# Kernel optimization log

Measured on AMD Instinct MI355X. Metric: run time of the kernel, lower is better.

The kernel has to match this reference:

```python
import jax, jax.numpy as jnp
import numpy as np

B, N = 64, 4096
D_IN, D_SLOT, K, N_ITER, MLP_H = 128, 128, 8, 3, 256
EPS = 1e-8
LN_EPS = 1e-5  # torch LayerNorm default


def layer_norm(x, g, b):
    m = jnp.mean(x, axis=-1, keepdims=True)
    v = jnp.mean((x - m) ** 2, axis=-1, keepdims=True)
    return (x - m) * jax.lax.rsqrt(v + LN_EPS) * g + b


def setup_inputs() -> dict:
    key = jax.random.key(0)
    ks = jax.random.split(key, 12)
    s = D_SLOT ** -0.5
    return {
        "inputs": jax.random.normal(ks[0], (B, N, D_IN), jnp.float32),
        "noise": jax.random.normal(ks[1], (B, K, D_SLOT), jnp.float32),
        "ln_in_g": jnp.ones((D_IN,), jnp.float32),
        "ln_in_b": jnp.zeros((D_IN,), jnp.float32),
        "ln_sl_g": jnp.ones((D_SLOT,), jnp.float32),
        "ln_sl_b": jnp.zeros((D_SLOT,), jnp.float32),
        "ln_mlp_g": jnp.ones((D_SLOT,), jnp.float32),
        "ln_mlp_b": jnp.zeros((D_SLOT,), jnp.float32),
        "slots_mu": jax.random.normal(ks[2], (1, 1, D_SLOT), jnp.float32) * s,
        "slots_log_sigma": jnp.zeros((1, 1, D_SLOT), jnp.float32),
        "Wq": jax.random.normal(ks[3], (D_SLOT, D_SLOT), jnp.float32) * s,
        "Wk": jax.random.normal(ks[4], (D_SLOT, D_IN), jnp.float32) * s,
        "Wv": jax.random.normal(ks[5], (D_SLOT, D_IN), jnp.float32) * s,
        "gru_Wih": jax.random.normal(ks[6], (3 * D_SLOT, D_SLOT), jnp.float32) * s,
        "gru_Whh": jax.random.normal(ks[7], (3 * D_SLOT, D_SLOT), jnp.float32) * s,
        "gru_bih": jnp.zeros((3 * D_SLOT,), jnp.float32),
        "gru_bhh": jnp.zeros((3 * D_SLOT,), jnp.float32),
        "mlp_W1": jax.random.normal(ks[8], (MLP_H, D_SLOT), jnp.float32) * s,
        "mlp_b1": jnp.zeros((MLP_H,), jnp.float32),
        "mlp_W2": jax.random.normal(ks[9], (D_SLOT, MLP_H), jnp.float32) * (MLP_H ** -0.5),
        "mlp_b2": jnp.zeros((D_SLOT,), jnp.float32),
    }


def gru_cell(x, h, Wih, Whh, bih, bhh):
    # torch GRUCell: gate order r, z, n
    gx = x @ Wih.T + bih
    gh = h @ Whh.T + bhh
    xr, xz, xn = jnp.split(gx, 3, axis=-1)
    hr, hz, hn = jnp.split(gh, 3, axis=-1)
    r = jax.nn.sigmoid(xr + hr)
    z = jax.nn.sigmoid(xz + hz)
    n = jnp.tanh(xn + r * hn)
    return (1.0 - z) * n + z * h


def reference(inputs, noise, ln_in_g, ln_in_b, ln_sl_g, ln_sl_b, ln_mlp_g, ln_mlp_b,
              slots_mu, slots_log_sigma, Wq, Wk, Wv,
              gru_Wih, gru_Whh, gru_bih, gru_bhh,
              mlp_W1, mlp_b1, mlp_W2, mlp_b2):
    # init slots: mu + sigma * eps
    slots = slots_mu + jnp.exp(slots_log_sigma) * noise  # (B, K, d)
    x = layer_norm(inputs, ln_in_g, ln_in_b)
    k = jnp.einsum('bnd,ed->bne', x, Wk)  # (B, N, d_slot)
    v = jnp.einsum('bnd,ed->bne', x, Wv)
    scale = D_SLOT ** -0.5
    attn = None
    for _ in range(N_ITER):
        slots_prev = slots
        s_n = layer_norm(slots, ln_sl_g, ln_sl_b)
        q = jnp.einsum('bkd,ed->bke', s_n, Wq)
        dots = jnp.einsum('bkd,bnd->bkn', q, k) * scale
        attn = jax.nn.softmax(dots, axis=1)  # competitive: softmax over slots
        attn_normed = attn / (jnp.sum(attn, axis=-1, keepdims=True) + EPS)
        updates = jnp.einsum('bkn,bnd->bkd', attn_normed, v)
        slots = gru_cell(updates.reshape(-1, D_SLOT), slots_prev.reshape(-1, D_SLOT),
                         gru_Wih, gru_Whh, gru_bih, gru_bhh).reshape(B, K, D_SLOT)
        h = layer_norm(slots, ln_mlp_g, ln_mlp_b)
        h = jax.nn.gelu(h @ mlp_W1.T + mlp_b1, approximate=False)
        slots = slots + h @ mlp_W2.T + mlp_b2
    return slots, attn
```

## Files before the change

### kernel.cpp

```cpp
#include <hip/hip_runtime.h>
#include <hip/hip_bf16.h>
#include <math.h>

typedef unsigned int u32;
typedef unsigned long long u64;
typedef unsigned short u16;
typedef __bf16 bf16x8 __attribute__((ext_vector_type(8)));
typedef float f32x4 __attribute__((ext_vector_type(4)));

#define DEV __device__ __forceinline__

DEV u32 bfr(float f){ u32 u = __float_as_uint(f); return (u + 0x7fffu + ((u>>16)&1u)) >> 16; }
DEV u16 b1v(float a){ return __builtin_bit_cast(u16, (__bf16)a); }
DEV u32 pk2(float a, float b){
  return (u32)__builtin_bit_cast(u16, (__bf16)a) | ((u32)__builtin_bit_cast(u16, (__bf16)b) << 16);
}
DEV float red32(float v){
  v += __shfl_xor(v,1); v += __shfl_xor(v,2); v += __shfl_xor(v,4);
  v += __shfl_xor(v,8); v += __shfl_xor(v,16); return v;
}

__global__ void kInitSlots(const float* __restrict__ noise, const float* __restrict__ mu,
                           const float* __restrict__ ls, float* __restrict__ slots){
  int i4 = blockIdx.x*256 + threadIdx.x;
  int d4 = i4 & 31;
  float4 nv = ((const float4*)noise)[i4];
  float4 mv = ((const float4*)mu)[d4];
  float4 lv = ((const float4*)ls)[d4];
  float4 r;
  r.x = mv.x + expf(lv.x)*nv.x;
  r.y = mv.y + expf(lv.y)*nv.y;
  r.z = mv.z + expf(lv.z)*nv.z;
  r.w = mv.w + expf(lv.w)*nv.w;
  ((float4*)slots)[i4] = r;
}

__global__ void kInitW(const float* __restrict__ Wk, const float* __restrict__ Wv,
                       const float* __restrict__ g, const float* __restrict__ bb,
                       u16* __restrict__ wg, float* __restrict__ c1, float* __restrict__ c2){
  int e = threadIdx.x;
  const float4* src = (const float4*)((e < 128) ? (Wk + e*128) : (Wv + (e-128)*128));
  float a1 = 0.f, a2 = 0.f;
  #pragma unroll
  for (int d4 = 0; d4 < 32; ++d4){
    float4 wv = src[d4];
    float4 gv = ((const float4*)g)[d4];
    float4 bv = ((const float4*)bb)[d4];
    a1 += wv.x*gv.x + wv.y*gv.y + wv.z*gv.z + wv.w*gv.w;
    a2 += wv.x*bv.x + wv.y*bv.y + wv.z*bv.z + wv.w*bv.w;
    u32 w0 = bfr(wv.x*gv.x) | (bfr(wv.y*gv.y) << 16);
    u32 w1 = bfr(wv.z*gv.z) | (bfr(wv.w*gv.w) << 16);
    *(uint2*)&wg[e*128 + d4*4] = make_uint2(w0, w1);
  }
  c1[e] = a1; c2[e] = a2;
}

__global__ void kInitT(const float* __restrict__ Wih, const float* __restrict__ Whh,
                       const float* __restrict__ W1, const float* __restrict__ W2,
                       float2* __restrict__ gruT, float* __restrict__ w1T, float* __restrict__ w2T){
  int i = blockIdx.x*256 + threadIdx.x;
  if (i < 49152){
    int d = i / 384, g = i - d*384;
    gruT[i] = make_float2(Wih[g*128 + d], Whh[g*128 + d]);
  } else if (i < 81920){
    int j = i - 49152;
    int d = j >> 8, h = j & 255;
    w1T[j] = W1[h*128 + d];
  } else if (i < 114688){
    int q = i - 81920;
    int j = q >> 7, d = q & 127;
    w2T[q] = W2[d*256 + j];
  }
}

__global__ __launch_bounds__(512, 2) void kA(const float* __restrict__ x,
    const u16* __restrict__ wg, const float* __restrict__ c1g, const float* __restrict__ c2g,
    u16* __restrict__ kbuf, u16* __restrict__ vbuf)
{
  __shared__ __align__(16) u16 sWg[128*128];
  __shared__ __align__(16) u16 sE[8*16*128];
  __shared__ float sC1[128], sC2[128];
  const int t = threadIdx.x, l = t & 63, w = t >> 6;
  const int bid = blockIdx.x;
  const int half = (bid >> 3) & 1;
  const int sub  = (bid >> 4) & 1;
  const int rowgroup = (bid & 7)*32 + (bid >> 5);
  const int rowbase = rowgroup * 1024;

  const uint4* wg4 = (const uint4*)wg;
  #pragma unroll
  for (int p = 0; p < 4; ++p){
    int G = t + p*512;
    int row = G >> 4, g = G & 15;
    uint4 v = wg4[(half*128 + row)*16 + g];
    *(uint4*)&sWg[row*128 + ((g ^ (row & 7)) << 3)] = v;
  }
  if (t < 128){ sC1[t] = c1g[half*128 + t]; sC2[t] = c2g[half*128 + t]; }
  __syncthreads();

  u16* dstbuf = half ? vbuf : kbuf;
  const float4* x4 = (const float4*)x;

  #pragma unroll 1
  for (int s = sub*4; s < sub*4 + 4; ++s){
    const int r0 = rowbase + s*128 + w*16;
    const int myrow = r0 + (l & 15);
    float s1 = 0.f, s2 = 0.f;
    uint4 af[4];
    #pragma unroll
    for (int kt = 0; kt < 4; ++kt){
      int g = kt*4 + (l >> 4);
      float4 A = x4[(size_t)myrow*32 + g*2];
      float4 B = x4[(size_t)myrow*32 + g*2 + 1];
      s1 += A.x + A.y + A.z + A.w + B.x + B.y + B.z + B.w;
      s2 += A.x*A.x + A.y*A.y + A.z*A.z + A.w*A.w
          + B.x*B.x + B.y*B.y + B.z*B.z + B.w*B.w;
      af[kt].x = pk2(A.x, A.y);
      af[kt].y = pk2(A.z, A.w);
      af[kt].z = pk2(B.x, B.y);
      af[kt].w = pk2(B.z, B.w);
    }
    s1 += __shfl_xor(s1, 16); s2 += __shfl_xor(s2, 16);
    s1 += __shfl_xor(s1, 32); s2 += __shfl_xor(s2, 32);
    float m = s1 * 0.0078125f;
    float rstd = rsqrtf(s2 * 0.0078125f - m*m + 1e-5f);
    f32x4 acc[8];
    #pragma unroll
    for (int c_ = 0; c_ < 8; ++c_) acc[c_] = (f32x4){0.f,0.f,0.f,0.f};
    #pragma unroll
    for (int ct = 0; ct < 8; ++ct){
      uint4 bf[4];
      #pragma unroll
      for (int kt = 0; kt < 4; ++kt){
        int wr = ct*16 + (l & 15);
        int g = kt*4 + (l >> 4);
        bf[kt] = *(const uint4*)&sWg[wr*128 + ((g ^ (wr & 7)) << 3)];
      }
      #pragma unroll
      for (int kt = 0; kt < 4; ++kt)
        acc[ct] = __builtin_amdgcn_mfma_f32_16x16x32_bf16(
            __builtin_bit_cast(bf16x8, af[kt]),
            __builtin_bit_cast(bf16x8, bf[kt]),
            acc[ct], 0, 0, 0);
    }
    float mvp[4], rvp[4];
    #pragma unroll
    for (int r = 0; r < 4; ++r){
      int rl = (l >> 4)*4 + r;
      mvp[r] = __shfl(m, rl);
      rvp[r] = __shfl(rstd, rl);
    }
    #pragma unroll
    for (int ct = 0; ct < 8; ++ct){
      int col = ct*16 + (l & 15);
      float c1v = sC1[col], c2v = sC2[col];
      #pragma unroll
      for (int r = 0; r < 4; ++r){
        int rl = (l >> 4)*4 + r;
        float valf = rvp[r]*(acc[ct][r] - mvp[r]*c1v) + c2v;
        int gran = (col >> 3) ^ (rl & 7);
        sE[w*2048 + rl*128 + (gran << 3) + (col & 7)] = b1v(valf);
      }
    }
    uint4* dst4 = (uint4*)dstbuf;
    #pragma unroll
    for (int p = 0; p < 4; ++p){
      int fl = l + p*64;
      int nl = fl >> 4, gb = fl & 15;
      uint4 v = *(const uint4*)&sE[w*2048 + nl*128 + ((gb ^ (nl & 7)) << 3)];
      dst4[(size_t)(r0 + nl)*16 + gb] = v;
    }
  }
}

__global__ __launch_bounds__(256) void kQ(const float* __restrict__ slots,
    const float* __restrict__ Wq, const float* __restrict__ lng, const float* __restrict__ lnb,
    uint4* __restrict__ qg)
{
  const int b = blockIdx.x, t = threadIdx.x;
  const int k8 = t >> 5, q32 = t & 31;
  __shared__ __align__(16) float sSn[1024];
  __shared__ __align__(16) float sQ[1024];
  {
    float4 sv = ((const float4*)slots)[b*256 + t];
    float s  = sv.x + sv.y + sv.z + sv.w;
    float ss = sv.x*sv.x + sv.y*sv.y + sv.z*sv.z + sv.w*sv.w;
    s = red32(s); ss = red32(ss);
    float m = s*0.0078125f, var = ss*0.0078125f - m*m;
    float rstd = rsqrtf(var + 1e-5f);
    float4 gv = ((const float4*)lng)[q32], bv = ((const float4*)lnb)[q32];
    float4 sn;
    sn.x = (sv.x - m)*rstd*gv.x + bv.x;
    sn.y = (sv.y - m)*rstd*gv.y + bv.y;
    sn.z = (sv.z - m)*rstd*gv.z + bv.z;
    sn.w = (sv.w - m)*rstd*gv.w + bv.w;
    *(float4*)&sSn[t*4] = sn;
  }
  __syncthreads();
  {
    const float4* Wq4 = (const float4*)Wq;
    #pragma unroll
    for (int i = 0; i < 4; ++i){
      int e = i*32 + q32;
      float acc = 0.f;
      #pragma unroll
      for (int d4 = 0; d4 < 32; ++d4){
        float4 qs = *(const float4*)&sSn[k8*128 + d4*4];
        float4 wv = Wq4[e*32 + d4];
        acc = fmaf(qs.x,wv.x,acc); acc = fmaf(qs.y,wv.y,acc);
        acc = fmaf(qs.z,wv.z,acc); acc = fmaf(qs.w,wv.w,acc);
      }
      sQ[k8*128 + e] = acc * 0.08838834764831845f;
    }
  }
  __syncthreads();
  if (t < 128){
    int slot = t >> 4, g = t & 15;
    const float* src = &sQ[slot*128 + g*8];
    uint4 o;
    o.x = pk2(src[0], src[1]); o.y = pk2(src[2], src[3]);
    o.z = pk2(src[4], src[5]); o.w = pk2(src[6], src[7]);
    qg[(b*8 + slot)*16 + g] = o;
  }
}

__global__ __launch_bounds__(256) void kB(const u16* __restrict__ kbuf,
   const u16* __restrict__ vbuf, const uint4* __restrict__ qg,
   float* __restrict__ part, float* __restrict__ attn_out, int write_attn,
   int cshift, int ntiles)
{
  const int t = threadIdx.x;
  const int b = blockIdx.x >> cshift, chunk = blockIdx.x & ((1 << cshift) - 1);
  const int w = t >> 6, l = t & 63;
  __shared__ __align__(16) u16 sVT[128*64];
  __shared__ __align__(16) u16 sAttnB[16*64];
  __shared__ float sRsP[32];

  uint4 qf[4];
  {
    int slot = l & 15;
    uint4 z = make_uint4(0,0,0,0);
    qf[0] = z; qf[1] = z; qf[2] = z; qf[3] = z;
    if (slot < 8){
      const uint4* qb = qg + ((size_t)b*8 + slot)*16 + (l >> 4);
      #pragma unroll
      for (int kt = 0; kt < 4; ++kt) qf[kt] = qb[kt*4];
    }
  }

  f32x4 accPV0 = (f32x4){0.f,0.f,0.f,0.f};
  f32x4 accPV1 = (f32x4){0.f,0.f,0.f,0.f};
  float rs = 0.f;
  const int myrow = w*16 + (l & 15);
  const size_t base = (size_t)b*4096 + (size_t)chunk*(ntiles*64);

  uint4 kf[4], vld[4];
  {
    const u16* kr = kbuf + (base + myrow)*128;
    #pragma unroll
    for (int kt = 0; kt < 4; ++kt) kf[kt] = *(const uint4*)(kr + (kt*4 + (l >> 4))*8);
    const uint4* vg = (const uint4*)(vbuf + base*128);
    #pragma unroll
    for (int p = 0; p < 4; ++p) vld[p] = vg[t + p*256];
  }

  #pragma unroll 1
  for (int tile = 0; tile < ntiles; ++tile){
    const int n0 = tile*64;
    f32x4 dacc = (f32x4){0.f,0.f,0.f,0.f};
    #pragma unroll
    for (int kt = 0; kt < 4; ++kt)
      dacc = __builtin_amdgcn_mfma_f32_16x16x32_bf16(
          __builtin_bit_cast(bf16x8, kf[kt]),
          __builtin_bit_cast(bf16x8, qf[kt]), dacc, 0, 0, 0);
    uint4 vldN[4];
    if (tile < ntiles - 1){
      const u16* kr = kbuf + (base + n0 + 64 + myrow)*128;
      #pragma unroll
      for (int kt = 0; kt < 4; ++kt) kf[kt] = *(const uint4*)(kr + (kt*4 + (l >> 4))*8);
      const uint4* vg = (const uint4*)(vbuf + (base + n0 + 64)*128);
      #pragma unroll
      for (int p = 0; p < 4; ++p) vldN[p] = vg[t + p*256];
    }
    float at[4];
    #pragma unroll
    for (int r = 0; r < 4; ++r){
      float d = dacc[r];
      float mx = fmaxf(d, __shfl_xor(d, 1));
      mx = fmaxf(mx, __shfl_xor(mx, 2));
      mx = fmaxf(mx, __shfl_xor(mx, 4));
      float e = expf(d - mx);
      float ssum = e + __shfl_xor(e, 1);
      ssum += __shfl_xor(ssum, 2);
      ssum += __shfl_xor(ssum, 4);
      at[r] = e / ssum;
      rs += at[r];
    }
    {
      int slot = l & 15;
      int nb = w*16 + (l >> 4)*4;
      int g = (nb >> 3) ^ (slot & 7);
      *(u64*)((char*)sAttnB + slot*128 + (g << 4) + ((nb & 7) << 1)) =
          ((u64)pk2(at[2], at[3]) << 32) | (u64)pk2(at[0], at[1]);
    }
    #pragma unroll
    for (int p = 0; p < 4; ++p){
      int fl = t + p*256;
      int nl = fl >> 4, gb = fl & 15;
      u32 arr[4] = {vld[p].x, vld[p].y, vld[p].z, vld[p].w};
      #pragma unroll
      for (int h = 0; h < 4; ++h){
        #pragma unroll
        for (int e2 = 0; e2 < 2; ++e2){
          int e = h*2 + e2;
          int d = gb*8 + e;
          int g = (nl >> 3) ^ (d & 7) ^ (gb & 7);
          *(u16*)((char*)sVT + d*128 + (g << 4) + ((nl & 7) << 1)) =
              (u16)(e2 ? (arr[h] >> 16) : (arr[h] & 0xffffu));
        }
      }
    }
    if (write_attn && (l & 15) < 8){
      #pragma unroll
      for (int r = 0; r < 4; ++r)
        attn_out[(size_t)(b*8 + (l & 15))*4096 + chunk*(ntiles*64) + n0 + w*16 + (l >> 4)*4 + r] = at[r];
    }
    __syncthreads();
    #pragma unroll
    for (int step = 0; step < 2; ++step){
      uint4 paf;
      {
        int slot = l & 15;
        int g = (step*4 + (l >> 4)) ^ (slot & 7);
        paf = *(const uint4*)((const char*)sAttnB + slot*128 + (g << 4));
      }
      #pragma unroll
      for (int ct = 0; ct < 2; ++ct){
        int d = w*32 + ct*16 + (l & 15);
        int g = (step*4 + (l >> 4)) ^ (d & 7) ^ ((d >> 3) & 7);
        uint4 pbf = *(const uint4*)((const char*)sVT + d*128 + (g << 4));
        if (ct == 0)
          accPV0 = __builtin_amdgcn_mfma_f32_16x16x32_bf16(
              __builtin_bit_cast(bf16x8, paf), __builtin_bit_cast(bf16x8, pbf), accPV0, 0,0,0);
        else
          accPV1 = __builtin_amdgcn_mfma_f32_16x16x32_bf16(
              __builtin_bit_cast(bf16x8, paf), __builtin_bit_cast(bf16x8, pbf), accPV1, 0,0,0);
      }
    }
    __syncthreads();
    if (tile < ntiles - 1){
      #pragma unroll
      for (int p = 0; p < 4; ++p) vld[p] = vldN[p];
    }
  }

  float* pb = part + (size_t)blockIdx.x*1040;
  if ((l >> 4) < 2){
    #pragma unroll
    for (int r = 0; r < 4; ++r){
      int slot = (l >> 4)*4 + r;
      pb[slot*128 + w*32 + (l & 15)] = accPV0[r];
      pb[slot*128 + w*32 + 16 + (l & 15)] = accPV1[r];
    }
  }
  rs += __shfl_xor(rs, 16);
  rs += __shfl_xor(rs, 32);
  if (l < 8) sRsP[w*8 + l] = rs;
  __syncthreads();
  if (t < 8) pb[1024 + t] = sRsP[t] + sRsP[8 + t] + sRsP[16 + t] + sRsP[24 + t];
}

__global__ __launch_bounds__(384) void kC(const float* __restrict__ part,
  float* __restrict__ slots, const float2* __restrict__ gruT,
  const float* __restrict__ bih, const float* __restrict__ bhh,
  const float* __restrict__ lng, const float* __restrict__ lnb,
  const float* __restrict__ w1T, const float* __restrict__ b1,
  const float* __restrict__ w2T, const float* __restrict__ b2,
  const float* __restrict__ lnslg, const float* __restrict__ lnslb,
  const float* __restrict__ Wq, uint4* __restrict__ qg,
  float* __restrict__ out_slots, int last, int nchunk)
{
  const int t = threadIdx.x;
  const int r = blockIdx.x, b = r >> 3, k = r & 7;
  __shared__ float sU[128], sS[128], sG1[384], sG2[384];
  __shared__ float sNew[128], sH[128], sH1[256];
  __shared__ float sP[4];

  if (t < 128){
    float rs = 1e-8f;
    for (int c = 0; c < nchunk; ++c) rs += part[(size_t)(b*nchunk + c)*1040 + 1024 + k];
    float u = 0.f;
    for (int c = 0; c < nchunk; ++c) u += part[(size_t)(b*nchunk + c)*1040 + k*128 + t];
    sU[t] = u / rs;
    sS[t] = slots[r*128 + t];
  }
  __syncthreads();

  {
    float acc1 = bih[t], acc2 = bhh[t];
    #pragma unroll 8
    for (int d = 0; d < 128; ++d){
      float2 w = gruT[d*384 + t];
      float ud = sU[d], sd = sS[d];
      acc1 = fmaf(ud, w.x, acc1);
      acc2 = fmaf(sd, w.y, acc2);
    }
    sG1[t] = acc1; sG2[t] = acc2;
  }
  __syncthreads();

  if (t < 128){
    float rr = 1.f/(1.f + expf(-(sG1[t] + sG2[t])));
    float zz = 1.f/(1.f + expf(-(sG1[128 + t] + sG2[128 + t])));
    float nn = tanhf(sG1[256 + t] + rr*sG2[256 + t]);
    sNew[t] = (1.f - zz)*nn + zz*sS[t];
  }
  __syncthreads();
  if (t < 128){
    float v = sNew[t];
    float s = v, ss = v*v;
    s  += __shfl_xor(s,1);  ss += __shfl_xor(ss,1);
    s  += __shfl_xor(s,2);  ss += __shfl_xor(ss,2);
    s  += __shfl_xor(s,4);  ss += __shfl_xor(ss,4);
    s  += __shfl_xor(s,8);  ss += __shfl_xor(ss,8);
    s  += __shfl_xor(s,16); ss += __shfl_xor(ss,16);
    s  += __shfl_xor(s,32); ss += __shfl_xor(ss,32);
    if ((t & 63) == 0){ sP[(t >> 6)*2] = s; sP[(t >> 6)*2 + 1] = ss; }
  }
  __syncthreads();
  if (t < 128){
    float s = sP[0] + sP[2], ss = sP[1] + sP[3];
    float m = s*0.0078125f, var = ss*0.0078125f - m*m;
    float rstd = rsqrtf(var + 1e-5f);
    sH[t] = (sNew[t] - m)*rstd*lng[t] + lnb[t];
  }
  __syncthreads();

  if (t < 256){
    float acc = b1[t];
    #pragma unroll 8
    for (int d = 0; d < 128; ++d)
      acc = fmaf(sH[d], w1T[d*256 + t], acc);
    sH1[t] = 0.5f*acc*(1.f + erff(acc*0.70710678118654752f));
  }
  __syncthreads();

  float res = 0.f;
  if (t < 128){
    float acc = b2[t];
    #pragma unroll 8
    for (int j = 0; j < 256; ++j)
      acc = fmaf(sH1[j], w2T[j*128 + t], acc);
    res = sNew[t] + acc;
    slots[r*128 + t] = res;
    if (last) out_slots[r*128 + t] = res;
  }
  if (last) return;

  __syncthreads();
  if (t < 128) sH[t] = res;
  __syncthreads();
  if (t < 128){
    float v = sH[t];
    float s = v, ss = v*v;
    s  += __shfl_xor(s,1);  ss += __shfl_xor(ss,1);
    s  += __shfl_xor(s,2);  ss += __shfl_xor(ss,2);
    s  += __shfl_xor(s,4);  ss += __shfl_xor(ss,4);
    s  += __shfl_xor(s,8);  ss += __shfl_xor(ss,8);
    s  += __shfl_xor(s,16); ss += __shfl_xor(ss,16);
    s  += __shfl_xor(s,32); ss += __shfl_xor(ss,32);
    if ((t & 63) == 0){ sP[(t >> 6)*2] = s; sP[(t >> 6)*2 + 1] = ss; }
  }
  __syncthreads();
  if (t < 128){
    float s = sP[0] + sP[2], ss = sP[1] + sP[3];
    float m = s*0.0078125f, var = ss*0.0078125f - m*m;
    float rstd = rsqrtf(var + 1e-5f);
    sU[t] = (sH[t] - m)*rstd*lnslg[t] + lnslb[t];
  }
  __syncthreads();
  if (t < 128){
    const float4* Wq4 = (const float4*)Wq;
    float acc = 0.f;
    #pragma unroll 8
    for (int d4 = 0; d4 < 32; ++d4){
      float4 wv = Wq4[t*32 + d4];
      float4 hv = *(const float4*)&sU[d4*4];
      acc = fmaf(wv.x,hv.x,acc); acc = fmaf(wv.y,hv.y,acc);
      acc = fmaf(wv.z,hv.z,acc); acc = fmaf(wv.w,hv.w,acc);
    }
    sG1[t] = acc * 0.08838834764831845f;
  }
  __syncthreads();
  if (t < 16){
    const float* src = &sG1[t*8];
    uint4 o;
    o.x = pk2(src[0], src[1]); o.y = pk2(src[2], src[3]);
    o.z = pk2(src[4], src[5]); o.w = pk2(src[6], src[7]);
    qg[(size_t)r*16 + t] = o;
  }
}

extern "C" void kernel_launch(void* const* d_in, const int* in_sizes, int n_in,
                              void* d_out, int out_size, void* d_ws, size_t ws_size,
                              hipStream_t stream)
{
  const float* inputs   = (const float*)d_in[0];
  const float* noise    = (const float*)d_in[1];
  const float* ln_in_g  = (const float*)d_in[2];
  const float* ln_in_b  = (const float*)d_in[3];
  const float* ln_sl_g  = (const float*)d_in[4];
  const float* ln_sl_b  = (const float*)d_in[5];
  const float* ln_mlp_g = (const float*)d_in[6];
  const float* ln_mlp_b = (const float*)d_in[7];
  const float* slots_mu = (const float*)d_in[8];
  const float* slots_ls = (const float*)d_in[9];
  const float* Wq  = (const float*)d_in[10];
  const float* Wk  = (const float*)d_in[11];
  const float* Wv  = (const float*)d_in[12];
  const float* Wih = (const float*)d_in[13];
  const float* Whh = (const float*)d_in[14];
  const float* bih = (const float*)d_in[15];
  const float* bhh = (const float*)d_in[16];
  const float* W1  = (const float*)d_in[17];
  const float* b1  = (const float*)d_in[18];
  const float* W2  = (const float*)d_in[19];
  const float* b2  = (const float*)d_in[20];
  float* out = (float*)d_out;

  char* ws = (char*)d_ws;
  u16*   kbuf  = (u16*)ws;
  u16*   vbuf  = (u16*)(ws + 67108864);
  float* slots = (float*)(ws + 134217728);
  u16*   wg    = (u16*)(ws + 134479872);
  float* c1    = (float*)(ws + 134545408);
  float* c2    = (float*)(ws + 134546432);
  float* part  = (float*)(ws + 134547456);

  int cshift, nchunk;
  {
    size_t need16 = 134547456ull + 16ull*64*1040*4 + 393216 + 131072 + 131072 + 131072;
    if (ws_size >= need16){ cshift = 4; nchunk = 16; }
    else                  { cshift = 3; nchunk = 8;  }
  }
  size_t partB = (size_t)nchunk*64*1040*4;
  float2* gruT = (float2*)(ws + 134547456 + partB);
  float*  w1T  = (float*)(ws + 134547456 + partB + 393216);
  float*  w2T  = (float*)(ws + 134547456 + partB + 393216 + 131072);
  uint4*  qg   = (uint4*)(ws + 134547456 + partB + 393216 + 262144);
  int ntiles = 64 / nchunk;

  kInitSlots<<<64, 256, 0, stream>>>(noise, slots_mu, slots_ls, slots);
  kInitW<<<1, 256, 0, stream>>>(Wk, Wv, ln_in_g, ln_in_b, wg, c1, c2);
  kInitT<<<448, 256, 0, stream>>>(Wih, Whh, W1, W2, gruT, w1T, w2T);
  kA<<<1024, 512, 0, stream>>>(inputs, wg, c1, c2, kbuf, vbuf);
  kQ<<<64, 256, 0, stream>>>(slots, Wq, ln_sl_g, ln_sl_b, qg);
  for (int it = 0; it < 3; ++it){
    kB<<<64*nchunk, 256, 0, stream>>>(kbuf, vbuf, qg, part, out + 65536,
                                      it == 2, cshift, ntiles);
    kC<<<512, 384, 0, stream>>>(part, slots, gruT, bih, bhh,
                                ln_mlp_g, ln_mlp_b, w1T, b1, w2T, b2,
                                ln_sl_g, ln_sl_b, Wq, qg, out, it == 2, nchunk);
  }
}
```

Measured before the change: 317.8 us.

## Double-buffer LDS tiles in attention kernel to drop second barrier; widen x loads

The attention/PV kernel now keeps two copies of the transposed-V and attention tiles in shared memory, alternating per tile. This allows the trailing per-tile __syncthreads to be removed, leaving one barrier per iteration and a single barrier after the loop. Separately, the K/V projection kernel reorders its k-dimension mapping so each lane reads and writes contiguous 16-byte chunks, and the weight prep packs 8 bf16 per store. The changes use more LDS per block, which may lower occupancy, and the k reorder must stay consistent between weights and activations.

```diff
diff --git a/kernel.cpp b/kernel.cpp
--- a/kernel.cpp
+++ b/kernel.cpp
@@ -40,17 +40,26 @@
                        u16* __restrict__ wg, float* __restrict__ c1, float* __restrict__ c2){
   int e = threadIdx.x;
   const float4* src = (const float4*)((e < 128) ? (Wk + e*128) : (Wv + (e-128)*128));
+  const float4* g4 = (const float4*)g;
+  const float4* b4 = (const float4*)bb;
   float a1 = 0.f, a2 = 0.f;
   #pragma unroll
-  for (int d4 = 0; d4 < 32; ++d4){
-    float4 wv = src[d4];
-    float4 gv = ((const float4*)g)[d4];
-    float4 bv = ((const float4*)bb)[d4];
-    a1 += wv.x*gv.x + wv.y*gv.y + wv.z*gv.z + wv.w*gv.w;
-    a2 += wv.x*bv.x + wv.y*bv.y + wv.z*bv.z + wv.w*bv.w;
-    u32 w0 = bfr(wv.x*gv.x) | (bfr(wv.y*gv.y) << 16);
-    u32 w1 = bfr(wv.z*gv.z) | (bfr(wv.w*gv.w) << 16);
-    *(uint2*)&wg[e*128 + d4*4] = make_uint2(w0, w1);
+  for (int gr = 0; gr < 16; ++gr){
+    int kt = gr >> 2, h = gr & 3;
+    int iA = kt*8 + h, iB = kt*8 + 4 + h;
+    float4 wa = src[iA], wb = src[iB];
+    float4 ga = g4[iA], gb = g4[iB];
+    float4 ba = b4[iA], bbv = b4[iB];
+    a1 += wa.x*ga.x + wa.y*ga.y + wa.z*ga.z + wa.w*ga.w
+        + wb.x*gb.x + wb.y*gb.y + wb.z*gb.z + wb.w*gb.w;
+    a2 += wa.x*ba.x + wa.y*ba.y + wa.z*ba.z + wa.w*ba.w
+        + wb.x*bbv.x + wb.y*bbv.y + wb.z*bbv.z + wb.w*bbv.w;
+    uint4 o;
+    o.x = pk2(wa.x*ga.x, wa.y*ga.y);
+    o.y = pk2(wa.z*ga.z, wa.w*ga.w);
+    o.z = pk2(wb.x*gb.x, wb.y*gb.y);
+    o.w = pk2(wb.z*gb.z, wb.w*gb.w);
+    *(uint4*)&wg[e*128 + gr*8] = o;
   }
   c1[e] = a1; c2[e] = a2;
 }
@@ -105,13 +114,13 @@
   for (int s = sub*4; s < sub*4 + 4; ++s){
     const int r0 = rowbase + s*128 + w*16;
     const int myrow = r0 + (l & 15);
+    const int h = l >> 4;
     float s1 = 0.f, s2 = 0.f;
     uint4 af[4];
     #pragma unroll
     for (int kt = 0; kt < 4; ++kt){
-      int g = kt*4 + (l >> 4);
-      float4 A = x4[(size_t)myrow*32 + g*2];
-      float4 B = x4[(size_t)myrow*32 + g*2 + 1];
+      float4 A = x4[(size_t)myrow*32 + kt*8 + h];
+      float4 B = x4[(size_t)myrow*32 + kt*8 + 4 + h];
       s1 += A.x + A.y + A.z + A.w + B.x + B.y + B.z + B.w;
       s2 += A.x*A.x + A.y*A.y + A.z*A.z + A.w*A.w
           + B.x*B.x + B.y*B.y + B.z*B.z + B.w*B.w;
@@ -133,7 +142,7 @@
       #pragma unroll
       for (int kt = 0; kt < 4; ++kt){
         int wr = ct*16 + (l & 15);
-        int g = kt*4 + (l >> 4);
+        int g = kt*4 + h;
         bf[kt] = *(const uint4*)&sWg[wr*128 + ((g ^ (wr & 7)) << 3)];
       }
       #pragma unroll
@@ -146,7 +155,7 @@
     float mvp[4], rvp[4];
     #pragma unroll
     for (int r = 0; r < 4; ++r){
-      int rl = (l >> 4)*4 + r;
+      int rl = h*4 + r;
       mvp[r] = __shfl(m, rl);
       rvp[r] = __shfl(rstd, rl);
     }
@@ -156,7 +165,7 @@
       float c1v = sC1[col], c2v = sC2[col];
       #pragma unroll
       for (int r = 0; r < 4; ++r){
-        int rl = (l >> 4)*4 + r;
+        int rl = h*4 + r;
         float valf = rvp[r]*(acc[ct][r] - mvp[r]*c1v) + c2v;
         int gran = (col >> 3) ^ (rl & 7);
         sE[w*2048 + rl*128 + (gran << 3) + (col & 7)] = b1v(valf);
@@ -232,8 +241,8 @@
   const int t = threadIdx.x;
   const int b = blockIdx.x >> cshift, chunk = blockIdx.x & ((1 << cshift) - 1);
   const int w = t >> 6, l = t & 63;
-  __shared__ __align__(16) u16 sVT[128*64];
-  __shared__ __align__(16) u16 sAttnB[16*64];
+  __shared__ __align__(16) u16 sVT[2][128*64];
+  __shared__ __align__(16) u16 sAttnB[2][16*64];
   __shared__ float sRsP[32];
 
   uint4 qf[4];
@@ -264,8 +273,9 @@
     for (int p = 0; p < 4; ++p) vld[p] = vg[t + p*256];
   }
 
-  #pragma unroll 1
+  #pragma unroll 2
   for (int tile = 0; tile < ntiles; ++tile){
+    const int cur = tile & 1;
     const int n0 = tile*64;
     f32x4 dacc = (f32x4){0.f,0.f,0.f,0.f};
     #pragma unroll
@@ -300,7 +310,7 @@
       int slot = l & 15;
       int nb = w*16 + (l >> 4)*4;
       int g = (nb >> 3) ^ (slot & 7);
-      *(u64*)((char*)sAttnB + slot*128 + (g << 4) + ((nb & 7) << 1)) =
+      *(u64*)((char*)sAttnB[cur] + slot*128 + (g << 4) + ((nb & 7) << 1)) =
           ((u64)pk2(at[2], at[3]) << 32) | (u64)pk2(at[0], at[1]);
     }
     #pragma unroll
@@ -309,14 +319,14 @@
       int nl = fl >> 4, gb = fl & 15;
       u32 arr[4] = {vld[p].x, vld[p].y, vld[p].z, vld[p].w};
       #pragma unroll
-      for (int h = 0; h < 4; ++h){
+      for (int hh = 0; hh < 4; ++hh){
         #pragma unroll
         for (int e2 = 0; e2 < 2; ++e2){
-          int e = h*2 + e2;
+          int e = hh*2 + e2;
           int d = gb*8 + e;
           int g = (nl >> 3) ^ (d & 7) ^ (gb & 7);
-          *(u16*)((char*)sVT + d*128 + (g << 4) + ((nl & 7) << 1)) =
-              (u16)(e2 ? (arr[h] >> 16) : (arr[h] & 0xffffu));
+          *(u16*)((char*)sVT[cur] + d*128 + (g << 4) + ((nl & 7) << 1)) =
+              (u16)(e2 ? (arr[hh] >> 16) : (arr[hh] & 0xffffu));
         }
       }
     }
@@ -332,13 +342,13 @@
       {
         int slot = l & 15;
         int g = (step*4 + (l >> 4)) ^ (slot & 7);
-        paf = *(const uint4*)((const char*)sAttnB + slot*128 + (g << 4));
+        paf = *(const uint4*)((const char*)sAttnB[cur] + slot*128 + (g << 4));
       }
       #pragma unroll
       for (int ct = 0; ct < 2; ++ct){
         int d = w*32 + ct*16 + (l & 15);
         int g = (step*4 + (l >> 4)) ^ (d & 7) ^ ((d >> 3) & 7);
-        uint4 pbf = *(const uint4*)((const char*)sVT + d*128 + (g << 4));
+        uint4 pbf = *(const uint4*)((const char*)sVT[cur] + d*128 + (g << 4));
         if (ct == 0)
           accPV0 = __builtin_amdgcn_mfma_f32_16x16x32_bf16(
               __builtin_bit_cast(bf16x8, paf), __builtin_bit_cast(bf16x8, pbf), accPV0, 0,0,0);
@@ -347,13 +357,13 @@
               __builtin_bit_cast(bf16x8, paf), __builtin_bit_cast(bf16x8, pbf), accPV1, 0,0,0);
       }
     }
-    __syncthreads();
     if (tile < ntiles - 1){
       #pragma unroll
       for (int p = 0; p < 4; ++p) vld[p] = vldN[p];
     }
   }
 
+  __syncthreads();
   float* pb = part + (size_t)blockIdx.x*1040;
   if ((l >> 4) < 2){
     #pragma unroll
```

Result: no change. 315.3 us (-0.8%).
